# Performance work log

Measured on AMD Instinct MI355X. Metric: run time of the kernel, lower is better.

## Reference

```python
import jax, jax.numpy as jnp
import numpy as np

# ---- static config ----
B, H, W, C = 32, 64, 64, 256
WS, SHIFT, NH = 8, 4, 8
HD = C // NH
N = WS * WS  # tokens per window
NW = (H // WS) * (W // WS)
EPS = 1e-5


def _relative_position_index(ws):
    ch, cw = np.meshgrid(np.arange(ws), np.arange(ws), indexing='ij')
    coords = np.stack([ch, cw]).reshape(2, -1)          # (2, N)
    rel = coords[:, :, None] - coords[:, None, :]        # (2, N, N)
    rel = rel.transpose(1, 2, 0)
    rel[:, :, 0] += ws - 1
    rel[:, :, 1] += ws - 1
    rel[:, :, 0] *= 2 * ws - 1
    return jnp.asarray(rel.sum(-1))                      # (N, N) int


def _shifted_window_mask(h, w, ws, shift):
    img = np.zeros((h, w))
    slices = (slice(0, -ws), slice(-ws, -shift), slice(-shift, None))
    cnt = 0
    for hs in slices:
        for wsl in slices:
            img[hs, wsl] = cnt
            cnt += 1
    mw = img.reshape(h // ws, ws, w // ws, ws).transpose(0, 2, 1, 3).reshape(-1, ws * ws)
    diff = mw[:, None, :] - mw[:, :, None]
    return jnp.asarray(np.where(diff != 0, -100.0, 0.0).astype(np.float32))  # (nW, N, N)


REL_IDX = _relative_position_index(WS)
ATTN_MASK = _shifted_window_mask(H, W, WS, SHIFT)


def _layernorm(x, g, b):
    mu = jnp.mean(x, axis=-1, keepdims=True)
    var = jnp.mean(jnp.square(x - mu), axis=-1, keepdims=True)
    return (x - mu) * jax.lax.rsqrt(var + EPS) * g + b


def _window_partition(x):  # (B,H,W,C) -> (B*nW, N, C)
    x = x.reshape(B, H // WS, WS, W // WS, WS, C)
    return x.transpose(0, 1, 3, 2, 4, 5).reshape(-1, N, C)


def _window_reverse(win):  # (B*nW, N, C) -> (B,H,W,C)
    x = win.reshape(B, H // WS, W // WS, WS, WS, C)
    return x.transpose(0, 1, 3, 2, 4, 5).reshape(B, H, W, C)


def setup_inputs() -> dict:
    key = jax.random.key(0)
    ks = jax.random.split(key, 6)
    s = lambda fan_in: 1.0 / np.sqrt(fan_in)
    return {
        'x': jax.random.normal(ks[0], (B, H * W, C), jnp.float32),
        'norm1_g': jnp.ones((C,), jnp.float32),
        'norm1_b': jnp.zeros((C,), jnp.float32),
        'qkv_w': jax.random.normal(ks[1], (C, 3 * C), jnp.float32) * s(C),
        'qkv_b': jnp.zeros((3 * C,), jnp.float32),
        'proj_w': jax.random.normal(ks[2], (C, C), jnp.float32) * s(C),
        'proj_b': jnp.zeros((C,), jnp.float32),
        'bias_table': jax.random.normal(ks[3], ((2 * WS - 1) ** 2, NH), jnp.float32) * 0.02,
        'norm2_g': jnp.ones((C,), jnp.float32),
        'norm2_b': jnp.zeros((C,), jnp.float32),
        'fc1_w': jax.random.normal(ks[4], (C, 4 * C), jnp.float32) * s(C),
        'fc1_b': jnp.zeros((4 * C,), jnp.float32),
        'fc2_w': jax.random.normal(ks[5], (4 * C, C), jnp.float32) * s(4 * C),
        'fc2_b': jnp.zeros((C,), jnp.float32),
    }


def reference(x, norm1_g, norm1_b, qkv_w, qkv_b, proj_w, proj_b, bias_table,
              norm2_g, norm2_b, fc1_w, fc1_b, fc2_w, fc2_b):
    shortcut = x
    h = _layernorm(x, norm1_g, norm1_b).reshape(B, H, W, C)
    # cyclic shift
    h = jnp.roll(h, shift=(-SHIFT, -SHIFT), axis=(1, 2))
    xw = _window_partition(h)                               # (Bw, N, C), Bw = B*nW
    # window attention
    qkv = xw @ qkv_w + qkv_b                                 # (Bw, N, 3C)
    qkv = qkv.reshape(-1, N, 3, NH, HD).transpose(2, 0, 3, 1, 4)
    q, k, v = qkv[0], qkv[1], qkv[2]                         # (Bw, NH, N, HD)
    attn = jnp.einsum('whnd,whmd->whnm', q * (HD ** -0.5), k)
    rpb = bias_table[REL_IDX.reshape(-1)].reshape(N, N, NH).transpose(2, 0, 1)
    attn = attn + rpb[None]
    attn = attn.reshape(B, NW, NH, N, N) + ATTN_MASK[None, :, None]
    attn = jax.nn.softmax(attn.reshape(-1, NH, N, N), axis=-1)
    out = jnp.einsum('whnm,whmd->whnd', attn, v)
    out = out.transpose(0, 2, 1, 3).reshape(-1, N, C)
    out = out @ proj_w + proj_b
    # reverse windows + shift back
    h = _window_reverse(out)
    h = jnp.roll(h, shift=(SHIFT, SHIFT), axis=(1, 2)).reshape(B, H * W, C)
    x = shortcut + h
    # MLP with pre-norm residual
    m = _layernorm(x, norm2_g, norm2_b)
    m = jax.nn.gelu(m @ fc1_w + fc1_b, approximate=False) @ fc2_w + fc2_b
    return x + m
```

## Files before the change

kernel.cpp:

```cpp
#include <hip/hip_runtime.h>
#include <hip/hip_bf16.h>


typedef __bf16 bf16;
typedef __bf16 bf16x8 __attribute__((ext_vector_type(8)));
typedef __bf16 bf16x4 __attribute__((ext_vector_type(4)));
typedef float  f32x4  __attribute__((ext_vector_type(4)));

#define M_TOK 131072

#define GLDS(gp, lp)                                                                   \
    __builtin_amdgcn_global_load_lds(                                                  \
        (const __attribute__((address_space(1))) unsigned int*)(gp),                   \
        (__attribute__((address_space(3))) unsigned int*)(lp), 16, 0, 0)

__global__ __launch_bounds__(256) void transpose_w(const float* __restrict__ src,
                                                   bf16* __restrict__ dst,
                                                   int K, int N) {
    int idx = blockIdx.x * 256 + threadIdx.x;
    int k = idx / N, n = idx - k * N;
    dst[(size_t)n * K + k] = (bf16)src[idx];
}

__global__ __launch_bounds__(256) void build_rpb(const float* __restrict__ bt,
                                                 float* __restrict__ rpb) {
    int idx = blockIdx.x * 256 + threadIdx.x;
    int h = idx >> 12, n = (idx >> 6) & 63, m = idx & 63;
    int ridx = ((n >> 3) - (m >> 3) + 7) * 15 + ((n & 7) - (m & 7) + 7);
    rpb[idx] = bt[ridx * 8 + h];
}

template <int PERM>
__global__ __launch_bounds__(256) void ln_k(const float* __restrict__ x,
                                            const float* __restrict__ g,
                                            const float* __restrict__ bb,
                                            bf16* __restrict__ dst) {
    int t = blockIdx.x * 4 + (threadIdx.x >> 6);
    int lane = threadIdx.x & 63;
    size_t src;
    if (PERM) {
        int w = t >> 6, n = t & 63;
        int b = w >> 6, nw = w & 63;
        int r = ((nw >> 3) * 8 + (n >> 3) + 4) & 63;
        int c = ((nw & 7) * 8 + (n & 7) + 4) & 63;
        src = ((size_t)b * 4096 + r * 64 + c) * 256;
    } else {
        src = (size_t)t * 256;
    }
    float4 v = *(const float4*)&x[src + lane * 4];
    float s = v.x + v.y + v.z + v.w;
    float sq = v.x * v.x + v.y * v.y + v.z * v.z + v.w * v.w;
#pragma unroll
    for (int off = 1; off < 64; off <<= 1) {
        s += __shfl_xor(s, off);
        sq += __shfl_xor(sq, off);
    }
    float mean = s * (1.0f / 256.0f);
    float var = sq * (1.0f / 256.0f) - mean * mean;
    float rstd = rsqrtf(var + 1e-5f);
    float4 gg = *(const float4*)&g[lane * 4];
    float4 bv = *(const float4*)&bb[lane * 4];
    bf16x4 o;
    o[0] = (bf16)((v.x - mean) * rstd * gg.x + bv.x);
    o[1] = (bf16)((v.y - mean) * rstd * gg.y + bv.y);
    o[2] = (bf16)((v.z - mean) * rstd * gg.z + bv.z);
    o[3] = (bf16)((v.w - mean) * rstd * gg.w + bv.w);
    *(bf16x4*)&dst[(size_t)t * 256 + lane * 4] = o;
}

__device__ __forceinline__ float fast_gelu(float v) {
    float t = v * v;
    float w = __builtin_fmaf(0.044715f * t, v, v);
    float e = __expf(-1.5957691216057308f * w);
    return v * __builtin_amdgcn_rcpf(1.0f + e);
}

template <int NDIM, int KDIM, int EPI>
__global__ __launch_bounds__(256) void gemm_k(const bf16* __restrict__ A,
                                              const bf16* __restrict__ Bt,
                                              const float* __restrict__ bias,
                                              bf16* __restrict__ outb,
                                              float* __restrict__ outf,
                                              const float* __restrict__ resid) {
    __shared__ __align__(16) bf16 SH[24576];
    constexpr int NBN = NDIM / 128;
    constexpr int NK = KDIM / 32;
    static_assert(NK >= 3, "pipeline needs >=3 K-steps");
    const int tid = threadIdx.x;
    const int nwg = gridDim.x;
    const int flat = blockIdx.x;
    const int cpx = nwg >> 3;
    const int orig = (flat & 7) * cpx + (flat >> 3);
    const int bm = orig / NBN, bn = orig % NBN;

    const int lane = tid & 63, wid = tid >> 6;
    const int wr = wid >> 1, wc = wid & 1;
    const int lhi = lane >> 4, llo = lane & 15;

    f32x4 acc[4][4];
#pragma unroll
    for (int i = 0; i < 4; i++)
#pragma unroll
        for (int j = 0; j < 4; j++) acc[i][j] = f32x4{0.f, 0.f, 0.f, 0.f};

    const int srow = wid * 32 + (lane >> 2);
    const int scol = (((lane & 3) - ((lane >> 3) & 3)) & 3) * 8;
    const bf16* Ap = A + (size_t)(bm * 128 + srow) * KDIM + scol;
    const bf16* Bp = Bt + (size_t)(bn * 128 + srow) * KDIM + scol;
    const int gsw = ((lhi + (llo >> 1)) & 3) * 8;

#define STAGE(bufidx)                                                                  \
    do {                                                                               \
        bf16* Al = SH + (bufidx)*4096 + wid * 1024;                                    \
        bf16* Bl = SH + 12288 + (bufidx)*4096 + wid * 1024;                            \
        GLDS(Ap, Al);                                                                  \
        GLDS(Ap + 16 * KDIM, Al + 16 * 32);                                            \
        GLDS(Bp, Bl);                                                                  \
        GLDS(Bp + 16 * KDIM, Bl + 16 * 32);                                            \
        Ap += 32;                                                                      \
        Bp += 32;                                                                      \
    } while (0)

#define COMPUTE(bufidx)                                                                \
    do {                                                                               \
        const int ab = (bufidx)*4096;                                                  \
        bf16x8 af[4], bfr[4];                                                          \
        _Pragma("unroll") for (int mi = 0; mi < 4; mi++) af[mi] =                      \
            *(const bf16x8*)&SH[ab + (wr * 64 + mi * 16 + llo) * 32 + gsw];            \
        _Pragma("unroll") for (int ni = 0; ni < 4; ni++) bfr[ni] =                     \
            *(const bf16x8*)&SH[12288 + ab + (wc * 64 + ni * 16 + llo) * 32 + gsw];    \
        _Pragma("unroll") for (int mi = 0; mi < 4; mi++)                               \
            _Pragma("unroll") for (int ni = 0; ni < 4; ni++) acc[mi][ni] =             \
                __builtin_amdgcn_mfma_f32_16x16x32_bf16(bfr[ni], af[mi],               \
                                                        acc[mi][ni], 0, 0, 0);         \
    } while (0)

#define WAITBAR(N)                                                                     \
    asm volatile("s_waitcnt vmcnt(" #N ")" ::: "memory");                              \
    __builtin_amdgcn_s_barrier();                                                      \
    __builtin_amdgcn_sched_barrier(0)

#define END_PHASE                                                                      \
    asm volatile("s_waitcnt lgkmcnt(0)" ::: "memory");                                 \
    __builtin_amdgcn_s_barrier();                                                      \
    __builtin_amdgcn_sched_barrier(0)

    STAGE(0);
    STAGE(1);
    STAGE(2);
    int buf = 0;
    for (int i = 0; i + 3 < NK; ++i) {
        WAITBAR(8);
        COMPUTE(buf);
        END_PHASE;
        STAGE(buf);
        buf = (buf == 2) ? 0 : buf + 1;
    }
    WAITBAR(8);
    COMPUTE(buf);
    buf = (buf == 2) ? 0 : buf + 1;
    WAITBAR(4);
    COMPUTE(buf);
    buf = (buf == 2) ? 0 : buf + 1;
    WAITBAR(0);
    COMPUTE(buf);

#undef STAGE
#undef COMPUTE
#undef WAITBAR
#undef END_PHASE

    __syncthreads();

    char* shb = (char*)SH;
    if constexpr (EPI == 0 || EPI == 2) {
#pragma unroll
        for (int ni = 0; ni < 4; ni++) {
            const int lcol = wc * 64 + ni * 16 + lhi * 4;
            const float4 b4 = *(const float4*)&bias[bn * 128 + lcol];
#pragma unroll
            for (int mi = 0; mi < 4; mi++) {
                const int ltok = wr * 64 + mi * 16 + llo;
                float v0 = acc[mi][ni][0] + b4.x;
                float v1 = acc[mi][ni][1] + b4.y;
                float v2 = acc[mi][ni][2] + b4.z;
                float v3 = acc[mi][ni][3] + b4.w;
                bf16x4 o;
                if constexpr (EPI == 2) {
                    o[0] = (bf16)fast_gelu(v0); o[1] = (bf16)fast_gelu(v1);
                    o[2] = (bf16)fast_gelu(v2); o[3] = (bf16)fast_gelu(v3);
                } else {
                    o[0] = (bf16)v0; o[1] = (bf16)v1; o[2] = (bf16)v2; o[3] = (bf16)v3;
                }
                const int u2 = (lcol >> 3) ^ (ltok & 15);
                *(bf16x4*)(shb + ltok * 256 + u2 * 16 + (lcol & 7) * 2) = o;
            }
        }
        __syncthreads();
        const int j = lane & 15;
#pragma unroll
        for (int rnd = 0; rnd < 8; rnd++) {
            const int ltok = wid * 32 + rnd * 4 + (lane >> 4);
            const int u2 = j ^ (ltok & 15);
            bf16x8 v = *(const bf16x8*)(shb + ltok * 256 + u2 * 16);
            *(bf16x8*)&outb[(size_t)(bm * 128 + ltok) * NDIM + bn * 128 + j * 8] = v;
        }
    } else {
#pragma unroll
        for (int p = 0; p < 2; p++) {
            if (wc == p) {
#pragma unroll
                for (int ni = 0; ni < 4; ni++) {
                    const int lcolh = ni * 16 + lhi * 4;
                    const float4 b4 = *(const float4*)&bias[bn * 128 + p * 64 + lcolh];
#pragma unroll
                    for (int mi = 0; mi < 4; mi++) {
                        const int ltok = wr * 64 + mi * 16 + llo;
                        float4 o = {acc[mi][ni][0] + b4.x, acc[mi][ni][1] + b4.y,
                                    acc[mi][ni][2] + b4.z, acc[mi][ni][3] + b4.w};
                        const int u2 = (lcolh >> 2) ^ (ltok & 15);
                        *(float4*)(shb + ltok * 256 + u2 * 16) = o;
                    }
                }
            }
            __syncthreads();
            const int j = lane & 15;
#pragma unroll
            for (int rnd = 0; rnd < 8; rnd++) {
                const int ltok = wid * 32 + rnd * 4 + (lane >> 4);
                const int u2 = j ^ (ltok & 15);
                float4 v = *(const float4*)(shb + ltok * 256 + u2 * 16);
                const int gcol = bn * 128 + p * 64 + j * 4;
                const int grow = bm * 128 + ltok;
                if constexpr (EPI == 1) {
                    int w = grow >> 6, n = grow & 63;
                    int b = w >> 6, nw = w & 63;
                    int rr = ((nw >> 3) * 8 + (n >> 3) + 4) & 63;
                    int cc = ((nw & 7) * 8 + (n & 7) + 4) & 63;
                    size_t dst = ((size_t)b * 4096 + rr * 64 + cc) * 256 + gcol;
                    float4 rs = *(const float4*)&resid[dst];
                    float4 o = {rs.x + v.x, rs.y + v.y, rs.z + v.z, rs.w + v.w};
                    *(float4*)&outf[dst] = o;
                } else {
                    size_t dst = (size_t)grow * NDIM + gcol;
                    float4 cur = *(const float4*)&outf[dst];
                    float4 o = {cur.x + v.x, cur.y + v.y, cur.z + v.z, cur.w + v.w};
                    *(float4*)&outf[dst] = o;
                }
            }
            if (p == 0) __syncthreads();
        }
    }
}

__device__ __forceinline__ int regid3(int p) { return p < 56 ? 0 : (p < 60 ? 1 : 2); }

__global__ __launch_bounds__(256) void attn_k(const bf16* __restrict__ qkv,
                                              const float* __restrict__ rpb,
                                              bf16* __restrict__ aout) {
    __shared__ __align__(16) bf16 Pl[4][64 * 80];
    const int wid = threadIdx.x >> 6, lane = threadIdx.x & 63;
    const int lhi = lane >> 4, llo = lane & 15;
    const int wh = blockIdx.x * 4 + wid;
    const int w = wh >> 3, h = wh & 7;
    const bf16* base = qkv + (size_t)w * (64 * 768);

    bf16x8 qf[4], kf[4];
#pragma unroll
    for (int i = 0; i < 4; i++)
        qf[i] = *(const bf16x8*)(base + (i * 16 + llo) * 768 + h * 32 + lhi * 8);
#pragma unroll
    for (int i = 0; i < 4; i++)
        kf[i] = *(const bf16x8*)(base + (i * 16 + llo) * 768 + 256 + h * 32 + lhi * 8);
    f32x4 s[4][4];
#pragma unroll
    for (int mi = 0; mi < 4; mi++)
#pragma unroll
        for (int ni = 0; ni < 4; ni++) {
            s[mi][ni] = f32x4{0.f, 0.f, 0.f, 0.f};
            s[mi][ni] =
                __builtin_amdgcn_mfma_f32_16x16x32_bf16(qf[mi], kf[ni], s[mi][ni], 0, 0, 0);
        }

    const int nw = w & 63;
    const int pr0 = (nw >> 3) * 8, pc0 = (nw & 7) * 8;
    int creg[4];
#pragma unroll
    for (int ni = 0; ni < 4; ni++) {
        int m = ni * 16 + llo;
        creg[ni] = regid3(pr0 + (m >> 3)) * 3 + regid3(pc0 + (m & 7));
    }
    float rmax[4][4], rsum[4][4];
#pragma unroll
    for (int mi = 0; mi < 4; mi++)
#pragma unroll
        for (int r = 0; r < 4; r++) {
            int n = mi * 16 + lhi * 4 + r;
            int rreg = regid3(pr0 + (n >> 3)) * 3 + regid3(pc0 + (n & 7));
            float mx = -1e30f;
#pragma unroll
            for (int ni = 0; ni < 4; ni++) {
                int m = ni * 16 + llo;
                float sv = s[mi][ni][r] * 0.17677669529663687f + rpb[(h * 64 + n) * 64 + m] +
                           (rreg == creg[ni] ? 0.0f : -100.0f);
                s[mi][ni][r] = sv;
                mx = fmaxf(mx, sv);
            }
            rmax[mi][r] = mx;
        }
#pragma unroll
    for (int off = 1; off < 16; off <<= 1)
#pragma unroll
        for (int mi = 0; mi < 4; mi++)
#pragma unroll
            for (int r = 0; r < 4; r++)
                rmax[mi][r] = fmaxf(rmax[mi][r], __shfl_xor(rmax[mi][r], off));
#pragma unroll
    for (int mi = 0; mi < 4; mi++)
#pragma unroll
        for (int r = 0; r < 4; r++) {
            float a = 0.f;
#pragma unroll
            for (int ni = 0; ni < 4; ni++) {
                float p = __expf(s[mi][ni][r] - rmax[mi][r]);
                s[mi][ni][r] = p;
                a += p;
            }
            rsum[mi][r] = a;
        }
#pragma unroll
    for (int off = 1; off < 16; off <<= 1)
#pragma unroll
        for (int mi = 0; mi < 4; mi++)
#pragma unroll
            for (int r = 0; r < 4; r++) rsum[mi][r] += __shfl_xor(rsum[mi][r], off);

    bf16* P = Pl[wid];
#pragma unroll
    for (int mi = 0; mi < 4; mi++)
#pragma unroll
        for (int r = 0; r < 4; r++) {
            float rinv = 1.0f / rsum[mi][r];
            int row = mi * 16 + lhi * 4 + r;
#pragma unroll
            for (int ni = 0; ni < 4; ni++)
                P[row * 80 + ni * 16 + llo] = (bf16)(s[mi][ni][r] * rinv);
        }

    f32x4 o[4][2];
#pragma unroll
    for (int mi = 0; mi < 4; mi++)
#pragma unroll
        for (int ni = 0; ni < 2; ni++) o[mi][ni] = f32x4{0.f, 0.f, 0.f, 0.f};
#pragma unroll
    for (int kc = 0; kc < 2; kc++) {
        bf16x8 pf[4], vf[2];
#pragma unroll
        for (int mi = 0; mi < 4; mi++)
            pf[mi] = *(const bf16x8*)(P + (mi * 16 + llo) * 80 + kc * 32 + lhi * 8);
#pragma unroll
        for (int ni = 0; ni < 2; ni++)
#pragma unroll
            for (int j = 0; j < 8; j++)
                vf[ni][j] = base[(kc * 32 + lhi * 8 + j) * 768 + 512 + h * 32 + ni * 16 + llo];
#pragma unroll
        for (int mi = 0; mi < 4; mi++)
#pragma unroll
            for (int ni = 0; ni < 2; ni++)
                o[mi][ni] =
                    __builtin_amdgcn_mfma_f32_16x16x32_bf16(pf[mi], vf[ni], o[mi][ni], 0, 0, 0);
    }
#pragma unroll
    for (int mi = 0; mi < 4; mi++)
#pragma unroll
        for (int ni = 0; ni < 2; ni++)
#pragma unroll
            for (int r = 0; r < 4; r++) {
                int row = mi * 16 + lhi * 4 + r;
                aout[(size_t)(w * 64 + row) * 256 + h * 32 + ni * 16 + llo] =
                    (bf16)o[mi][ni][r];
            }
}

extern "C" void kernel_launch(void* const* d_in, const int* in_sizes, int n_in,
                              void* d_out, int out_size, void* d_ws, size_t ws_size,
                              hipStream_t stream) {
    const float* x      = (const float*)d_in[0];
    const float* n1g    = (const float*)d_in[1];
    const float* n1b    = (const float*)d_in[2];
    const float* qkv_w  = (const float*)d_in[3];
    const float* qkv_b  = (const float*)d_in[4];
    const float* proj_w = (const float*)d_in[5];
    const float* proj_b = (const float*)d_in[6];
    const float* btab   = (const float*)d_in[7];
    const float* n2g    = (const float*)d_in[8];
    const float* n2b    = (const float*)d_in[9];
    const float* fc1_w  = (const float*)d_in[10];
    const float* fc1_b  = (const float*)d_in[11];
    const float* fc2_w  = (const float*)d_in[12];
    const float* fc2_b  = (const float*)d_in[13];
    float* out = (float*)d_out;
    char* ws = (char*)d_ws;

    constexpr size_t o_xw   = 0;
    constexpr size_t o_qkvb = 67108864ull;
    constexpr size_t o_attn = 268435456ull;
    constexpr size_t o_g    = 0;
    constexpr size_t o_h    = 268435456ull;
    constexpr size_t o_wq   = 335544320ull;
    constexpr size_t o_wp   = o_wq + 393216;
    constexpr size_t o_w1   = o_wp + 131072;
    constexpr size_t o_w2   = o_w1 + 524288;
    constexpr size_t o_rpb  = o_w2 + 524288;

    bf16* XW    = (bf16*)(ws + o_xw);
    bf16* QKVB  = (bf16*)(ws + o_qkvb);
    bf16* ATTN  = (bf16*)(ws + o_attn);
    bf16* Gbuf  = (bf16*)(ws + o_g);
    bf16* Hb    = (bf16*)(ws + o_h);
    bf16* WQ    = (bf16*)(ws + o_wq);
    bf16* WP    = (bf16*)(ws + o_wp);
    bf16* W1    = (bf16*)(ws + o_w1);
    bf16* W2    = (bf16*)(ws + o_w2);
    float* RPB  = (float*)(ws + o_rpb);

    dim3 blk(256);
    transpose_w<<<768, blk, 0, stream>>>(qkv_w, WQ, 256, 768);
    transpose_w<<<256, blk, 0, stream>>>(proj_w, WP, 256, 256);
    transpose_w<<<1024, blk, 0, stream>>>(fc1_w, W1, 256, 1024);
    transpose_w<<<1024, blk, 0, stream>>>(fc2_w, W2, 1024, 256);
    build_rpb<<<128, blk, 0, stream>>>(btab, RPB);

    ln_k<1><<<M_TOK / 4, blk, 0, stream>>>(x, n1g, n1b, XW);

    for (int c = 0; c < 4; ++c) {
        const size_t toff = (size_t)c * 32768;
        gemm_k<768, 256, 0><<<1536, blk, 0, stream>>>(XW + toff * 256, WQ, qkv_b,
                                                      QKVB, nullptr, nullptr);
        attn_k<<<1024, blk, 0, stream>>>(QKVB, RPB, ATTN + toff * 256);
    }

    gemm_k<256, 256, 1><<<2 * 1024, blk, 0, stream>>>(ATTN, WP, proj_b, nullptr, out, x);
    ln_k<0><<<M_TOK / 4, blk, 0, stream>>>(out, n2g, n2b, Hb);

    for (int q = 0; q < 4; ++q) {
        const size_t toff = (size_t)q * 32768;
        gemm_k<1024, 256, 2><<<2048, blk, 0, stream>>>(Hb + toff * 256, W1, fc1_b,
                                                       Gbuf, nullptr, nullptr);
        gemm_k<256, 1024, 3><<<512, blk, 0, stream>>>(Gbuf, W2, fc2_b, nullptr,
                                                      out + toff * 256, nullptr);
    }
}
```

Baseline: 584.9 us.

## Fuse projection GEMM, residual add and LayerNorm2 into one kernel

Adds a proj_ln_k kernel that computes the attention output projection over a 64-token by 256-column tile, so each block holds full rows. It then adds bias and the shifted-window residual, writes the fp32 output, and applies LayerNorm2 in the same pass, writing the bf16 normalized activations. This removes the separate LayerNorm launch and its re-read of the fp32 output. Hb moves to its own workspace region so it no longer aliases the attention buffer being read. The QKV/attention chunking also changes from four chunks to two larger ones, which means fewer launches in exchange for a larger intermediate buffer.

```diff
diff --git a/kernel.cpp b/kernel.cpp
--- a/kernel.cpp
+++ b/kernel.cpp
@@ -232,24 +232,154 @@
                 float4 v = *(const float4*)(shb + ltok * 256 + u2 * 16);
                 const int gcol = bn * 128 + p * 64 + j * 4;
                 const int grow = bm * 128 + ltok;
-                if constexpr (EPI == 1) {
-                    int w = grow >> 6, n = grow & 63;
-                    int b = w >> 6, nw = w & 63;
-                    int rr = ((nw >> 3) * 8 + (n >> 3) + 4) & 63;
-                    int cc = ((nw & 7) * 8 + (n & 7) + 4) & 63;
-                    size_t dst = ((size_t)b * 4096 + rr * 64 + cc) * 256 + gcol;
-                    float4 rs = *(const float4*)&resid[dst];
-                    float4 o = {rs.x + v.x, rs.y + v.y, rs.z + v.z, rs.w + v.w};
-                    *(float4*)&outf[dst] = o;
-                } else {
-                    size_t dst = (size_t)grow * NDIM + gcol;
-                    float4 cur = *(const float4*)&outf[dst];
-                    float4 o = {cur.x + v.x, cur.y + v.y, cur.z + v.z, cur.w + v.w};
-                    *(float4*)&outf[dst] = o;
-                }
+                size_t dst = (size_t)grow * NDIM + gcol;
+                float4 cur = *(const float4*)&outf[dst];
+                float4 o = {cur.x + v.x, cur.y + v.y, cur.z + v.z, cur.w + v.w};
+                *(float4*)&outf[dst] = o;
             }
             if (p == 0) __syncthreads();
         }
+    }
+}
+
+__global__ __launch_bounds__(256) void proj_ln_k(const bf16* __restrict__ A,
+                                                 const bf16* __restrict__ Bt,
+                                                 const float* __restrict__ bias,
+                                                 const float* __restrict__ resid,
+                                                 float* __restrict__ outf,
+                                                 const float* __restrict__ g2,
+                                                 const float* __restrict__ b2,
+                                                 bf16* __restrict__ hb) {
+    __shared__ __align__(16) bf16 SH[32768];
+    constexpr int KDIM = 256;
+    const int tid = threadIdx.x;
+    const int nwg = gridDim.x;
+    const int flat = blockIdx.x;
+    const int cpx = nwg >> 3;
+    const int bm = (flat & 7) * cpx + (flat >> 3);
+
+    const int lane = tid & 63, wid = tid >> 6;
+    const int lhi = lane >> 4, llo = lane & 15;
+
+    f32x4 acc[4][4];
+#pragma unroll
+    for (int i = 0; i < 4; i++)
+#pragma unroll
+        for (int j = 0; j < 4; j++) acc[i][j] = f32x4{0.f, 0.f, 0.f, 0.f};
+
+    const int scol = (((lane & 3) - ((lane >> 3) & 3)) & 3) * 8;
+    const bf16* Ap = A + (size_t)(bm * 64 + wid * 16 + (lane >> 2)) * KDIM + scol;
+    const bf16* Bp = Bt + (size_t)(wid * 64 + (lane >> 2)) * KDIM + scol;
+    const int gsw = ((lhi + (llo >> 1)) & 3) * 8;
+
+#define PSTAGE(bufidx)                                                                 \
+    do {                                                                               \
+        bf16* Al = SH + (bufidx)*2048 + wid * 512;                                     \
+        bf16* Bl = SH + 6144 + (bufidx)*8192 + wid * 2048;                             \
+        GLDS(Ap, Al);                                                                  \
+        GLDS(Bp, Bl);                                                                  \
+        GLDS(Bp + 16 * KDIM, Bl + 512);                                                \
+        GLDS(Bp + 32 * KDIM, Bl + 1024);                                               \
+        GLDS(Bp + 48 * KDIM, Bl + 1536);                                               \
+        Ap += 32;                                                                      \
+        Bp += 32;                                                                      \
+    } while (0)
+
+#define PCOMPUTE(bufidx)                                                               \
+    do {                                                                               \
+        bf16x8 af[4], bfr[4];                                                          \
+        _Pragma("unroll") for (int mi = 0; mi < 4; mi++) af[mi] =                      \
+            *(const bf16x8*)&SH[(bufidx)*2048 + (mi * 16 + llo) * 32 + gsw];           \
+        _Pragma("unroll") for (int ni = 0; ni < 4; ni++) bfr[ni] =                     \
+            *(const bf16x8*)&SH[6144 + (bufidx)*8192 +                                 \
+                                (wid * 64 + ni * 16 + llo) * 32 + gsw];                \
+        _Pragma("unroll") for (int mi = 0; mi < 4; mi++)                               \
+            _Pragma("unroll") for (int ni = 0; ni < 4; ni++) acc[mi][ni] =             \
+                __builtin_amdgcn_mfma_f32_16x16x32_bf16(bfr[ni], af[mi],               \
+                                                        acc[mi][ni], 0, 0, 0);         \
+    } while (0)
+
+#define PWAITBAR(N)                                                                    \
+    asm volatile("s_waitcnt vmcnt(" #N ")" ::: "memory");                              \
+    __builtin_amdgcn_s_barrier();                                                      \
+    __builtin_amdgcn_sched_barrier(0)
+
+    PSTAGE(0);
+    PSTAGE(1);
+    PSTAGE(2);
+    int buf = 0;
+    for (int i = 0; i + 3 < 8; ++i) {
+        PWAITBAR(10);
+        PCOMPUTE(buf);
+        asm volatile("s_waitcnt lgkmcnt(0)" ::: "memory");
+        __builtin_amdgcn_s_barrier();
+        __builtin_amdgcn_sched_barrier(0);
+        PSTAGE(buf);
+        buf = (buf == 2) ? 0 : buf + 1;
+    }
+    PWAITBAR(10);
+    PCOMPUTE(buf);
+    buf = (buf == 2) ? 0 : buf + 1;
+    PWAITBAR(5);
+    PCOMPUTE(buf);
+    buf = (buf == 2) ? 0 : buf + 1;
+    PWAITBAR(0);
+    PCOMPUTE(buf);
+
+#undef PSTAGE
+#undef PCOMPUTE
+#undef PWAITBAR
+
+    __syncthreads();
+
+    char* shb = (char*)SH;
+#pragma unroll
+    for (int ni = 0; ni < 4; ni++) {
+        const int col0 = wid * 64 + ni * 16 + lhi * 4;
+        const float4 b4 = *(const float4*)&bias[col0];
+#pragma unroll
+        for (int mi = 0; mi < 4; mi++) {
+            const int ltok = mi * 16 + llo;
+            float4 o = {acc[mi][ni][0] + b4.x, acc[mi][ni][1] + b4.y,
+                        acc[mi][ni][2] + b4.z, acc[mi][ni][3] + b4.w};
+            const int u2 = (col0 >> 2) ^ (ltok & 15);
+            *(float4*)(shb + ltok * 1024 + u2 * 16) = o;
+        }
+    }
+    __syncthreads();
+
+    const float4 gg = *(const float4*)&g2[lane * 4];
+    const float4 bb4 = *(const float4*)&b2[lane * 4];
+#pragma unroll
+    for (int rnd = 0; rnd < 16; rnd++) {
+        const int t = rnd * 4 + wid;
+        const int u2 = lane ^ (t & 15);
+        float4 v = *(const float4*)(shb + t * 1024 + u2 * 16);
+        const int grow = bm * 64 + t;
+        int w = grow >> 6, n = grow & 63;
+        int b = w >> 6, nw = w & 63;
+        int rr = ((nw >> 3) * 8 + (n >> 3) + 4) & 63;
+        int cc = ((nw & 7) * 8 + (n & 7) + 4) & 63;
+        const size_t rowbase = ((size_t)b * 4096 + rr * 64 + cc) * 256;
+        float4 rs = *(const float4*)&resid[rowbase + lane * 4];
+        float4 o = {rs.x + v.x, rs.y + v.y, rs.z + v.z, rs.w + v.w};
+        *(float4*)&outf[rowbase + lane * 4] = o;
+        float s = o.x + o.y + o.z + o.w;
+        float sq = o.x * o.x + o.y * o.y + o.z * o.z + o.w * o.w;
+#pragma unroll
+        for (int off = 1; off < 64; off <<= 1) {
+            s += __shfl_xor(s, off);
+            sq += __shfl_xor(sq, off);
+        }
+        float mean = s * (1.0f / 256.0f);
+        float var = sq * (1.0f / 256.0f) - mean * mean;
+        float rstd = rsqrtf(var + 1e-5f);
+        bf16x4 ho;
+        ho[0] = (bf16)((o.x - mean) * rstd * gg.x + bb4.x);
+        ho[1] = (bf16)((o.y - mean) * rstd * gg.y + bb4.y);
+        ho[2] = (bf16)((o.z - mean) * rstd * gg.z + bb4.z);
+        ho[3] = (bf16)((o.w - mean) * rstd * gg.w + bb4.w);
+        *(bf16x4*)&hb[rowbase + lane * 4] = ho;
     }
 }
 
@@ -407,7 +537,8 @@
     constexpr size_t o_attn = 268435456ull;
     constexpr size_t o_g    = 0;
     constexpr size_t o_h    = 268435456ull;
-    constexpr size_t o_wq   = 335544320ull;
+    constexpr size_t o_hb   = 335544320ull;
+    constexpr size_t o_wq   = o_hb + 67108864ull;
     constexpr size_t o_wp   = o_wq + 393216;
     constexpr size_t o_w1   = o_wp + 131072;
     constexpr size_t o_w2   = o_w1 + 524288;
@@ -417,7 +548,7 @@
     bf16* QKVB  = (bf16*)(ws + o_qkvb);
     bf16* ATTN  = (bf16*)(ws + o_attn);
     bf16* Gbuf  = (bf16*)(ws + o_g);
-    bf16* Hb    = (bf16*)(ws + o_h);
+    bf16* Hb    = (bf16*)(ws + o_hb);
     bf16* WQ    = (bf16*)(ws + o_wq);
     bf16* WP    = (bf16*)(ws + o_wp);
     bf16* W1    = (bf16*)(ws + o_w1);
@@ -433,15 +564,14 @@
 
     ln_k<1><<<M_TOK / 4, blk, 0, stream>>>(x, n1g, n1b, XW);
 
-    for (int c = 0; c < 4; ++c) {
-        const size_t toff = (size_t)c * 32768;
-        gemm_k<768, 256, 0><<<1536, blk, 0, stream>>>(XW + toff * 256, WQ, qkv_b,
+    for (int c = 0; c < 2; ++c) {
+        const size_t toff = (size_t)c * 65536;
+        gemm_k<768, 256, 0><<<3072, blk, 0, stream>>>(XW + toff * 256, WQ, qkv_b,
                                                       QKVB, nullptr, nullptr);
-        attn_k<<<1024, blk, 0, stream>>>(QKVB, RPB, ATTN + toff * 256);
-    }
-
-    gemm_k<256, 256, 1><<<2 * 1024, blk, 0, stream>>>(ATTN, WP, proj_b, nullptr, out, x);
-    ln_k<0><<<M_TOK / 4, blk, 0, stream>>>(out, n2g, n2b, Hb);
+        attn_k<<<2048, blk, 0, stream>>>(QKVB, RPB, ATTN + toff * 256);
+    }
+
+    proj_ln_k<<<2048, blk, 0, stream>>>(ATTN, WP, proj_b, x, out, n2g, n2b, Hb);
 
     for (int q = 0; q < 4; ++q) {
         const size_t toff = (size_t)q * 32768;
```

Result: no change. 590.4 us (+1.0%).
